# Kernel optimization log

Hardware: AMD Instinct MI355X
Metric: run time of the kernel (lower is better)

Reference implementation:

```python
import jax, jax.numpy as jnp
import numpy as np

TEMPERATURE = 0.07
C_MARGIN = 0.5
T_MARGIN = 1.0
GAMMA = 2.0
ALPHA = 0.25
SMOOTHING = 0.1
W_CONTRASTIVE = 0.1
W_TRIPLET = 0.1
W_FOCAL = 0.4
W_LABEL_SMOOTH = 0.4


def setup_inputs() -> dict:
    key = jax.random.key(0)
    k1, k2, k3 = jax.random.split(key, 3)
    B, C, D = 2048, 1000, 512
    pred = jax.random.normal(k1, (B, C), dtype=jnp.float32)
    target = jax.random.randint(k2, (B,), 0, C, dtype=jnp.int64)
    features = jax.random.normal(k3, (B, D), dtype=jnp.float32)
    return {"pred": pred, "target": target, "features": features}


def _safe_cdist(f):
    # Euclidean pairwise distance with zero-grad at zero distance (matches torch.cdist on diagonal).
    r = jnp.sum(f * f, axis=1)
    d2 = jnp.maximum(r[:, None] - 2.0 * (f @ f.T) + r[None, :], 0.0)
    pos = d2 > 0
    return jnp.sqrt(jnp.where(pos, d2, 1.0)) * pos


def _contrastive(features, labels):
    f = features / jnp.linalg.norm(features, axis=1, keepdims=True)
    sim = f @ f.T  # [B, B]
    lm = (labels[:, None] == labels[None, :]).astype(sim.dtype)
    pos = sim * lm
    pos_loss = -jnp.log(jnp.exp(pos / TEMPERATURE) + 1e-8)
    neg = sim * (1.0 - lm)
    neg_loss = jnp.maximum(C_MARGIN - neg, 0.0)
    return pos_loss.mean() + neg_loss.mean()


def _triplet(features, labels):
    B = features.shape[0]
    d = _safe_cdist(features)  # [B, B]
    lm = (labels[:, None] == labels[None, :]).astype(d.dtype)
    pm, nm = lm, 1.0 - lm

    def body(acc, args):
        di, pmi, nmi = args  # [B], [B], [B]
        # sum over (p, n): relu(d_ip - d_in + margin), masked
        contrib = jnp.sum(
            jnp.maximum(di[:, None] - di[None, :] + T_MARGIN, 0.0)
            * pmi[:, None] * nmi[None, :]
        )
        return acc + contrib, None

    loss, _ = jax.lax.scan(body, jnp.float32(0.0), (d, pm, nm))
    return loss / (B + 1e-8)


def _focal(pred, target):
    logp = jax.nn.log_softmax(pred, axis=1)
    ce = -jnp.take_along_axis(logp, target[:, None], axis=1)[:, 0]
    pt = jnp.exp(-ce)
    return (ALPHA * (1.0 - pt) ** GAMMA * ce).mean()


def _label_smoothing(pred, target):
    C = pred.shape[1]
    off = SMOOTHING / (C - 1)
    logp = jax.nn.log_softmax(pred, axis=1)
    # smooth target: off everywhere, (1 - smoothing) at target index
    tgt_logp = jnp.take_along_axis(logp, target[:, None], axis=1)[:, 0]
    loss = -(off * logp.sum(axis=1) + ((1.0 - SMOOTHING) - off) * tgt_logp)
    return loss.mean()


def reference(pred, target, features):
    lc = _contrastive(features, target)
    lt = _triplet(features, target)
    lf = _focal(pred, target)
    ls = _label_smoothing(pred, target)
    total = (W_CONTRASTIVE * lc + W_TRIPLET * lt
             + W_FOCAL * lf + W_LABEL_SMOOTH * ls)
    return jnp.stack([lc, lt, lf, ls, total])
```

## Files before the change

### kernel.cpp

```cpp
#include <hip/hip_runtime.h>
#include <hip/hip_bf16.h>
#include <math.h>

typedef __attribute__((ext_vector_type(8))) short bf16x8;
typedef __attribute__((ext_vector_type(4))) float f32x4;

static constexpr float TEMP_INV  = 1.0f / 0.07f;
static constexpr float C_MARGIN  = 0.5f;
static constexpr float T_MARGIN  = 1.0f;
static constexpr float ALPHA     = 0.25f;
static constexpr float SMOOTHING = 0.1f;
static constexpr float LSE_SHIFT = 8.0f;

__device__ __forceinline__ unsigned short f2bf(float x) {
    __hip_bfloat16 h = __float2bfloat16(x);
    return *reinterpret_cast<unsigned short*>(&h);
}
__device__ __forceinline__ float bf2f(unsigned short u) {
    union { unsigned int u32; float f; } U;
    U.u32 = ((unsigned int)u) << 16;
    return U.f;
}
__device__ __forceinline__ bf16x8 pack8(float4 a, float4 b) {
    bf16x8 r;
    r[0] = (short)f2bf(a.x); r[1] = (short)f2bf(a.y);
    r[2] = (short)f2bf(a.z); r[3] = (short)f2bf(a.w);
    r[4] = (short)f2bf(b.x); r[5] = (short)f2bf(b.y);
    r[6] = (short)f2bf(b.z); r[7] = (short)f2bf(b.w);
    return r;
}

__global__ __launch_bounds__(256) void gram_ce_kernel(
    const float* __restrict__ F, unsigned short* __restrict__ Gb,
    const float* __restrict__ pred, const int* __restrict__ target,
    float* __restrict__ partialCE, float* __restrict__ diag,
    float* __restrict__ inv_norm, int B, int D, int C, float off_const,
    int tilesX) {
    __shared__ unsigned short As[2][128 * 32];
    __shared__ unsigned short Bs[2][128 * 32];

    const int nTiles = tilesX * tilesX;
    const int tid = threadIdx.x;
    const int lane = tid & 63, wid = tid >> 6;

    if (blockIdx.x < nTiles) {
        const int b = blockIdx.x;
        const int x = b & 7, sq = x * 2 + ((b >> 3) >> 4);
        const int tis = (b >> 3) & 15;
        const int ti = (sq >> 2) * 4 + (tis >> 2);
        const int tj = (sq & 3) * 4 + (tis & 3);
        const int rowBase = ti * 128;
        const int colBase = tj * 128;
        const int wr = (wid >> 1) * 64;
        const int wc = (wid & 1) * 64;
        const int half = lane >> 4;
        const int rr   = lane & 15;

        const float* FA = F + (size_t)rowBase * D;
        const float* FB = F + (size_t)colBase * D;

        int ldo_[2]; size_t go_[2];
#pragma unroll
        for (int c = 0; c < 2; ++c) {
            const int chunk = c * 256 + tid;
            const int r2 = chunk >> 2, q = chunk & 3;
            ldo_[c] = r2 * 32 + ((q ^ (r2 & 3)) * 8);
            go_[c]  = (size_t)r2 * D + q * 8;
        }

        f32x4 acc[4][4];
#pragma unroll
        for (int m = 0; m < 4; ++m)
#pragma unroll
            for (int n = 0; n < 4; ++n) acc[m][n] = (f32x4){0.f, 0.f, 0.f, 0.f};

        float4 pa0[2], pa1[2], pb0[2], pb1[2];

#pragma unroll
        for (int c = 0; c < 2; ++c) {
            pa0[c] = *(const float4*)(FA + go_[c]);
            pa1[c] = *(const float4*)(FA + go_[c] + 4);
            pb0[c] = *(const float4*)(FB + go_[c]);
            pb1[c] = *(const float4*)(FB + go_[c] + 4);
        }
#pragma unroll
        for (int c = 0; c < 2; ++c) {
            *(bf16x8*)(&As[0][ldo_[c]]) = pack8(pa0[c], pa1[c]);
            *(bf16x8*)(&Bs[0][ldo_[c]]) = pack8(pb0[c], pb1[c]);
        }
        __syncthreads();

        const int NT = D / 32;
        for (int t = 0; t < NT; ++t) {
            const int cur = t & 1;
            if (t + 1 < NT) {
                const int k1 = (t + 1) * 32;
#pragma unroll
                for (int c = 0; c < 2; ++c) {
                    pa0[c] = *(const float4*)(FA + go_[c] + k1);
                    pa1[c] = *(const float4*)(FA + go_[c] + k1 + 4);
                    pb0[c] = *(const float4*)(FB + go_[c] + k1);
                    pb1[c] = *(const float4*)(FB + go_[c] + k1 + 4);
                }
            }
            bf16x8 af[4], bfv[4];
#pragma unroll
            for (int f = 0; f < 4; ++f) {
                const int ar = wr + f * 16 + rr;
                af[f]  = *(const bf16x8*)(&As[cur][ar * 32 + ((half ^ (ar & 3)) * 8)]);
                const int br = wc + f * 16 + rr;
                bfv[f] = *(const bf16x8*)(&Bs[cur][br * 32 + ((half ^ (br & 3)) * 8)]);
            }
#pragma unroll
            for (int m = 0; m < 4; ++m)
#pragma unroll
                for (int n = 0; n < 4; ++n)
                    acc[m][n] = __builtin_amdgcn_mfma_f32_16x16x32_bf16(
                        af[m], bfv[n], acc[m][n], 0, 0, 0);
            if (t + 1 < NT) {
#pragma unroll
                for (int c = 0; c < 2; ++c) {
                    *(bf16x8*)(&As[cur ^ 1][ldo_[c]]) = pack8(pa0[c], pa1[c]);
                    *(bf16x8*)(&Bs[cur ^ 1][ldo_[c]]) = pack8(pb0[c], pb1[c]);
                }
            }
            __syncthreads();
        }
#pragma unroll
        for (int m = 0; m < 4; ++m) {
            const int i0 = rowBase + wr + m * 16 + half * 4;
#pragma unroll
            for (int n = 0; n < 4; ++n) {
                const int j = colBase + wc + n * 16 + rr;
#pragma unroll
                for (int r = 0; r < 4; ++r)
                    Gb[(size_t)(i0 + r) * B + j] = f2bf(acc[m][n][r]);
            }
        }
    } else {
        const int i = (blockIdx.x - nTiles) * 4 + wid;
        const float4* Fr4 = (const float4*)(F + (size_t)i * D);
        float ns = 0.0f;
        for (int idx = lane; idx < (D >> 2); idx += 64) {
            float4 f = Fr4[idx];
            ns += f.x * f.x + f.y * f.y + f.z * f.z + f.w * f.w;
        }
        const float* prow = pred + (size_t)i * C;
        const float tlogit = prow[target[i]];
        const int Cv = C >> 2;
        float s = 0.0f, sp = 0.0f;
        for (int idx = lane; idx < Cv; idx += 64) {
            float4 v = ((const float4*)prow)[idx];
            s += __expf(v.x - LSE_SHIFT) + __expf(v.y - LSE_SHIFT)
               + __expf(v.z - LSE_SHIFT) + __expf(v.w - LSE_SHIFT);
            sp += v.x + v.y + v.z + v.w;
        }
        for (int j = Cv * 4 + lane; j < C; j += 64) {
            float v = prow[j];
            s += __expf(v - LSE_SHIFT);
            sp += v;
        }
#pragma unroll
        for (int off = 32; off > 0; off >>= 1) {
            s  += __shfl_down(s, off, 64);
            sp += __shfl_down(sp, off, 64);
            ns += __shfl_down(ns, off, 64);
        }
        if (lane == 0) {
            float lse = LSE_SHIFT + __logf(s);
            float tl  = tlogit - lse;
            float ce  = -tl;
            float pt  = __expf(tl);
            float omp = 1.0f - pt;
            float focal = ALPHA * omp * omp * ce;
            float sumlogp = sp - (float)C * lse;
            float lsv = -(off_const * sumlogp + ((1.0f - SMOOTHING) - off_const) * tl);
            partialCE[(size_t)i * 2]     = focal;
            partialCE[(size_t)i * 2 + 1] = lsv;
            diag[i] = ns;
            inv_norm[i] = 1.0f / sqrtf(ns);
        }
    }
}

__global__ __launch_bounds__(256) void row_loss_kernel(
    const unsigned short* __restrict__ Gb, const float* __restrict__ diag,
    const float* __restrict__ inv_norm, const int* __restrict__ labels,
    float* __restrict__ partial, int B) {
    __shared__ float p_d[256];
    __shared__ float red[12];
    __shared__ int p_cnt;
    const int tid = threadIdx.x;
    const int i = blockIdx.x;
    const int j0 = tid * 8;

    union { uint4 u; unsigned short s[8]; } GV;
    GV.u = *(const uint4*)(Gb + (size_t)i * B + j0);
    int lab[8];
    *(int4*)&lab[0] = *(const int4*)(labels + j0);
    *(int4*)&lab[4] = *(const int4*)(labels + j0 + 4);
    float dg[8], ivn[8];
    *(float4*)&dg[0]  = *(const float4*)(diag + j0);
    *(float4*)&dg[4]  = *(const float4*)(diag + j0 + 4);
    *(float4*)&ivn[0] = *(const float4*)(inv_norm + j0);
    *(float4*)&ivn[4] = *(const float4*)(inv_norm + j0 + 4);
    const int   li     = labels[i];
    const float ri     = diag[i];
    const float inv_ni = inv_norm[i];

    if (tid == 0) p_cnt = 0;
    __syncthreads();

    float pos = 0.0f, neg = 0.0f;
    float d8[8];
    int mmask = 0;
#pragma unroll
    for (int e = 0; e < 8; ++e) {
        const int j = j0 + e;
        const float g = bf2f(GV.s[e]);
        float sim = g * inv_ni * ivn[e];
        const float d2 = ri - 2.0f * g + dg[e];
        float d = (d2 > 0.0f) ? sqrtf(d2) : 0.0f;
        if (j == i) { sim = 1.0f; d = 0.0f; }
        d8[e] = d;
        if (lab[e] == li) {
            pos += -__logf(__expf(sim * TEMP_INV) + 1e-8f);
            neg += C_MARGIN;
            mmask |= (1 << e);
            int slot = atomicAdd(&p_cnt, 1);
            if (slot < 256) p_d[slot] = d;
        } else {
            neg += fmaxf(C_MARGIN - sim, 0.0f);
        }
    }
    __syncthreads();
    const int cnt = (p_cnt < 256) ? p_cnt : 256;
    float trip = 0.0f;
    for (int p = 0; p < cnt; ++p) {
        const float dp = p_d[p] + T_MARGIN;
#pragma unroll
        for (int e = 0; e < 8; ++e)
            if (!(mmask & (1 << e))) trip += fmaxf(dp - d8[e], 0.0f);
    }

    float r0 = pos, r1 = neg, r2 = trip;
#pragma unroll
    for (int off = 32; off > 0; off >>= 1) {
        r0 += __shfl_down(r0, off, 64);
        r1 += __shfl_down(r1, off, 64);
        r2 += __shfl_down(r2, off, 64);
    }
    const int lane = tid & 63, wid = tid >> 6;
    if (lane == 0) { red[wid] = r0; red[4 + wid] = r1; red[8 + wid] = r2; }
    __syncthreads();
    if (tid == 0) {
        float4 o;
        o.x = red[0] + red[1] + red[2] + red[3];
        o.y = red[4] + red[5] + red[6] + red[7];
        o.z = red[8] + red[9] + red[10] + red[11];
        o.w = 0.0f;
        *(float4*)(partial + (size_t)i * 4) = o;
    }
}

__global__ __launch_bounds__(1024) void reduce_kernel(
    const float* __restrict__ partialT, const float* __restrict__ partialCE,
    float* __restrict__ out, int B) {
    __shared__ float red[16][5];
    const int tid = threadIdx.x;
    float s[5] = {0.f, 0.f, 0.f, 0.f, 0.f};
    for (int r = tid; r < B; r += 1024) {
        float4 v = *(const float4*)(partialT + (size_t)r * 4);
        s[0] += v.x; s[1] += v.y; s[2] += v.z;
    }
    for (int t = tid; t < (B * 2) / 4; t += 1024) {
        float4 v = *(const float4*)(partialCE + (size_t)t * 4);
        s[3] += v.x + v.z; s[4] += v.y + v.w;
    }
#pragma unroll
    for (int off = 32; off > 0; off >>= 1) {
#pragma unroll
        for (int k = 0; k < 5; ++k) s[k] += __shfl_down(s[k], off, 64);
    }
    const int lane = tid & 63, wid = tid >> 6;
    if (lane == 0) {
#pragma unroll
        for (int k = 0; k < 5; ++k) red[wid][k] = s[k];
    }
    __syncthreads();
    if (tid == 0) {
        float t[5];
#pragma unroll
        for (int k = 0; k < 5; ++k) {
            t[k] = red[0][k];
#pragma unroll
            for (int q = 1; q < 16; ++q) t[k] += red[q][k];
        }
        double invB2 = 1.0 / ((double)B * (double)B);
        float lc = (float)(((double)t[0] + (double)t[1]) * invB2);
        float lt = (float)((double)t[2] / ((double)B + 1e-8));
        float lf = t[3] / (float)B;
        float ls = t[4] / (float)B;
        out[0] = lc;
        out[1] = lt;
        out[2] = lf;
        out[3] = ls;
        out[4] = 0.1f * lc + 0.1f * lt + 0.4f * lf + 0.4f * ls;
    }
}

extern "C" void kernel_launch(void* const* d_in, const int* in_sizes, int n_in,
                              void* d_out, int out_size, void* d_ws, size_t ws_size,
                              hipStream_t stream) {
    const float* pred     = (const float*)d_in[0];
    const int*   target   = (const int*)d_in[1];
    const float* features = (const float*)d_in[2];
    const int B = in_sizes[1];
    const int C = in_sizes[0] / B;
    const int D = in_sizes[2] / B;
    float* out = (float*)d_out;
    const int tilesX = B / 128;
    const int nTiles = tilesX * tilesX;

    float* partial   = (float*)d_ws;
    float* partialCE = partial + (size_t)B * 4;
    float* diag      = partialCE + (size_t)B * 2;
    float* inv_norm  = diag + B;
    unsigned short* Gb = (unsigned short*)(inv_norm + B);

    float off_const = SMOOTHING / (float)(C - 1);
    gram_ce_kernel<<<nTiles + B / 4, 256, 0, stream>>>(
        features, Gb, pred, target, partialCE, diag, inv_norm,
        B, D, C, off_const, tilesX);

    row_loss_kernel<<<B, 256, 0, stream>>>(Gb, diag, inv_norm, target,
                                           partial, B);

    reduce_kernel<<<1, 1024, 0, stream>>>(partial, partialCE, out, B);
}
```

Baseline: 31.17 us.

## Fuse norm, contrastive terms and distance computation into Gram GEMM epilogue

Each Gram tile now computes the squared row norms from the fp32 data it already loads for packing, then in the epilogue computes cosine similarity, the contrastive positive/negative sums and the Euclidean distance. It stores the bf16 distance matrix instead of the raw Gram matrix, with nontemporal stores. The row kernel now only does the triplet term and no longer reads diag/inv_norm arrays, and the separate norm pass in the CE blocks is removed. This moves transcendental work (exp, log, sqrt) into the GEMM blocks, adds shared-memory label/norm arrays and an extra block reduction there, and stores distance in bf16 rather than computing it from an fp32-derived Gram.

Result: slower. 37.99 us (+21.9%).

```diff
diff --git a/kernel.cpp b/kernel.cpp
--- a/kernel.cpp
+++ b/kernel.cpp
@@ -29,15 +29,20 @@
     r[6] = (short)f2bf(b.z); r[7] = (short)f2bf(b.w);
     return r;
 }
+__device__ __forceinline__ float dot4(float4 v) {
+    return v.x * v.x + v.y * v.y + v.z * v.z + v.w * v.w;
+}
 
 __global__ __launch_bounds__(256) void gram_ce_kernel(
-    const float* __restrict__ F, unsigned short* __restrict__ Gb,
+    const float* __restrict__ F, unsigned short* __restrict__ Gd,
     const float* __restrict__ pred, const int* __restrict__ target,
-    float* __restrict__ partialCE, float* __restrict__ diag,
-    float* __restrict__ inv_norm, int B, int D, int C, float off_const,
-    int tilesX) {
+    float* __restrict__ partialCE, float* __restrict__ partialPN,
+    int B, int D, int C, float off_const, int tilesX) {
     __shared__ unsigned short As[2][128 * 32];
     __shared__ unsigned short Bs[2][128 * 32];
+    __shared__ float rI[128], iI[128], rJ[128], iJ[128];
+    __shared__ int   labR[128], labC[128];
+    __shared__ float red[8];
 
     const int nTiles = tilesX * tilesX;
     const int tid = threadIdx.x;
@@ -59,6 +64,9 @@
         const float* FA = F + (size_t)rowBase * D;
         const float* FB = F + (size_t)colBase * D;
 
+        if (tid < 128) labR[tid] = target[rowBase + tid];
+        else           labC[tid - 128] = target[colBase + tid - 128];
+
         int ldo_[2]; size_t go_[2];
 #pragma unroll
         for (int c = 0; c < 2; ++c) {
@@ -74,6 +82,7 @@
 #pragma unroll
             for (int n = 0; n < 4; ++n) acc[m][n] = (f32x4){0.f, 0.f, 0.f, 0.f};
 
+        float nsA[2] = {0.f, 0.f}, nsB[2] = {0.f, 0.f};
         float4 pa0[2], pa1[2], pb0[2], pb1[2];
 
 #pragma unroll
@@ -87,6 +96,8 @@
         for (int c = 0; c < 2; ++c) {
             *(bf16x8*)(&As[0][ldo_[c]]) = pack8(pa0[c], pa1[c]);
             *(bf16x8*)(&Bs[0][ldo_[c]]) = pack8(pb0[c], pb1[c]);
+            nsA[c] += dot4(pa0[c]) + dot4(pa1[c]);
+            nsB[c] += dot4(pb0[c]) + dot4(pb1[c]);
         }
         __syncthreads();
 
@@ -122,29 +133,72 @@
                 for (int c = 0; c < 2; ++c) {
                     *(bf16x8*)(&As[cur ^ 1][ldo_[c]]) = pack8(pa0[c], pa1[c]);
                     *(bf16x8*)(&Bs[cur ^ 1][ldo_[c]]) = pack8(pb0[c], pb1[c]);
+                    nsA[c] += dot4(pa0[c]) + dot4(pa1[c]);
+                    nsB[c] += dot4(pb0[c]) + dot4(pb1[c]);
                 }
             }
             __syncthreads();
         }
+
+#pragma unroll
+        for (int c = 0; c < 2; ++c) {
+            float a = nsA[c], bb = nsB[c];
+            a  += __shfl_xor(a, 1, 64);  a  += __shfl_xor(a, 2, 64);
+            bb += __shfl_xor(bb, 1, 64); bb += __shfl_xor(bb, 2, 64);
+            if ((tid & 3) == 0) {
+                const int r = (c * 256 + tid) >> 2;
+                rI[r] = a;  iI[r] = 1.0f / sqrtf(a);
+                rJ[r] = bb; iJ[r] = 1.0f / sqrtf(bb);
+            }
+        }
+        __syncthreads();
+
+        float pos = 0.0f, neg = 0.0f;
+        int   jlab[4]; float jr[4], jij[4];
+#pragma unroll
+        for (int n = 0; n < 4; ++n) {
+            const int jl = wc + n * 16 + rr;
+            jlab[n] = labC[jl]; jr[n] = rJ[jl]; jij[n] = iJ[jl];
+        }
 #pragma unroll
         for (int m = 0; m < 4; ++m) {
-            const int i0 = rowBase + wr + m * 16 + half * 4;
-#pragma unroll
-            for (int n = 0; n < 4; ++n) {
-                const int j = colBase + wc + n * 16 + rr;
-#pragma unroll
-                for (int r = 0; r < 4; ++r)
-                    Gb[(size_t)(i0 + r) * B + j] = f2bf(acc[m][n][r]);
-            }
+#pragma unroll
+            for (int r = 0; r < 4; ++r) {
+                const int il = wr + m * 16 + half * 4 + r;
+                const int gi = rowBase + il;
+                const float ri_ = rI[il], ii = iI[il];
+                const int lr = labR[il];
+#pragma unroll
+                for (int n = 0; n < 4; ++n) {
+                    const int gj = colBase + wc + n * 16 + rr;
+                    const float g = acc[m][n][r];
+                    float sim = g * ii * jij[n];
+                    const float d2 = ri_ - 2.0f * g + jr[n];
+                    float d = (d2 > 0.0f) ? sqrtf(d2) : 0.0f;
+                    if (gi == gj) { sim = 1.0f; d = 0.0f; }
+                    if (lr == jlab[n]) {
+                        pos += -__logf(__expf(sim * TEMP_INV) + 1e-8f);
+                        neg += C_MARGIN;
+                    } else {
+                        neg += fmaxf(C_MARGIN - sim, 0.0f);
+                    }
+                    __builtin_nontemporal_store(f2bf(d), &Gd[(size_t)gi * B + gj]);
+                }
+            }
+        }
+#pragma unroll
+        for (int off = 32; off > 0; off >>= 1) {
+            pos += __shfl_down(pos, off, 64);
+            neg += __shfl_down(neg, off, 64);
+        }
+        if (lane == 0) { red[wid] = pos; red[4 + wid] = neg; }
+        __syncthreads();
+        if (tid == 0) {
+            partialPN[(size_t)b * 2]     = red[0] + red[1] + red[2] + red[3];
+            partialPN[(size_t)b * 2 + 1] = red[4] + red[5] + red[6] + red[7];
         }
     } else {
         const int i = (blockIdx.x - nTiles) * 4 + wid;
-        const float4* Fr4 = (const float4*)(F + (size_t)i * D);
-        float ns = 0.0f;
-        for (int idx = lane; idx < (D >> 2); idx += 64) {
-            float4 f = Fr4[idx];
-            ns += f.x * f.x + f.y * f.y + f.z * f.z + f.w * f.w;
-        }
         const float* prow = pred + (size_t)i * C;
         const float tlogit = prow[target[i]];
         const int Cv = C >> 2;
@@ -164,7 +218,6 @@
         for (int off = 32; off > 0; off >>= 1) {
             s  += __shfl_down(s, off, 64);
             sp += __shfl_down(sp, off, 64);
-            ns += __shfl_down(ns, off, 64);
         }
         if (lane == 0) {
             float lse = LSE_SHIFT + __logf(s);
@@ -177,60 +230,39 @@
             float lsv = -(off_const * sumlogp + ((1.0f - SMOOTHING) - off_const) * tl);
             partialCE[(size_t)i * 2]     = focal;
             partialCE[(size_t)i * 2 + 1] = lsv;
-            diag[i] = ns;
-            inv_norm[i] = 1.0f / sqrtf(ns);
         }
     }
 }
 
 __global__ __launch_bounds__(256) void row_loss_kernel(
-    const unsigned short* __restrict__ Gb, const float* __restrict__ diag,
-    const float* __restrict__ inv_norm, const int* __restrict__ labels,
+    const unsigned short* __restrict__ Gd, const int* __restrict__ labels,
     float* __restrict__ partial, int B) {
     __shared__ float p_d[256];
-    __shared__ float red[12];
+    __shared__ float red[4];
     __shared__ int p_cnt;
     const int tid = threadIdx.x;
     const int i = blockIdx.x;
     const int j0 = tid * 8;
 
     union { uint4 u; unsigned short s[8]; } GV;
-    GV.u = *(const uint4*)(Gb + (size_t)i * B + j0);
+    GV.u = *(const uint4*)(Gd + (size_t)i * B + j0);
     int lab[8];
     *(int4*)&lab[0] = *(const int4*)(labels + j0);
     *(int4*)&lab[4] = *(const int4*)(labels + j0 + 4);
-    float dg[8], ivn[8];
-    *(float4*)&dg[0]  = *(const float4*)(diag + j0);
-    *(float4*)&dg[4]  = *(const float4*)(diag + j0 + 4);
-    *(float4*)&ivn[0] = *(const float4*)(inv_norm + j0);
-    *(float4*)&ivn[4] = *(const float4*)(inv_norm + j0 + 4);
-    const int   li     = labels[i];
-    const float ri     = diag[i];
-    const float inv_ni = inv_norm[i];
+    const int li = labels[i];
 
     if (tid == 0) p_cnt = 0;
     __syncthreads();
 
-    float pos = 0.0f, neg = 0.0f;
     float d8[8];
     int mmask = 0;
 #pragma unroll
     for (int e = 0; e < 8; ++e) {
-        const int j = j0 + e;
-        const float g = bf2f(GV.s[e]);
-        float sim = g * inv_ni * ivn[e];
-        const float d2 = ri - 2.0f * g + dg[e];
-        float d = (d2 > 0.0f) ? sqrtf(d2) : 0.0f;
-        if (j == i) { sim = 1.0f; d = 0.0f; }
-        d8[e] = d;
+        d8[e] = bf2f(GV.s[e]);
         if (lab[e] == li) {
-            pos += -__logf(__expf(sim * TEMP_INV) + 1e-8f);
-            neg += C_MARGIN;
             mmask |= (1 << e);
             int slot = atomicAdd(&p_cnt, 1);
-            if (slot < 256) p_d[slot] = d;
-        } else {
-            neg += fmaxf(C_MARGIN - sim, 0.0f);
+            if (slot < 256) p_d[slot] = d8[e];
         }
     }
     __syncthreads();
@@ -243,35 +275,30 @@
             if (!(mmask & (1 << e))) trip += fmaxf(dp - d8[e], 0.0f);
     }
 
-    float r0 = pos, r1 = neg, r2 = trip;
-#pragma unroll
-    for (int off = 32; off > 0; off >>= 1) {
-        r0 += __shfl_down(r0, off, 64);
-        r1 += __shfl_down(r1, off, 64);
-        r2 += __shfl_down(r2, off, 64);
-    }
+#pragma unroll
+    for (int off = 32; off > 0; off >>= 1)
+        trip += __shfl_down(trip, off, 64);
     const int lane = tid & 63, wid = tid >> 6;
-    if (lane == 0) { red[wid] = r0; red[4 + wid] = r1; red[8 + wid] = r2; }
+    if (lane == 0) red[wid] = trip;
     __syncthreads();
-    if (tid == 0) {
-        float4 o;
-        o.x = red[0] + red[1] + red[2] + red[3];
-        o.y = red[4] + red[5] + red[6] + red[7];
-        o.z = red[8] + red[9] + red[10] + red[11];
-        o.w = 0.0f;
-        *(float4*)(partial + (size_t)i * 4) = o;
-    }
+    if (tid == 0)
+        partial[i] = red[0] + red[1] + red[2] + red[3];
 }
 
 __global__ __launch_bounds__(1024) void reduce_kernel(
-    const float* __restrict__ partialT, const float* __restrict__ partialCE,
-    float* __restrict__ out, int B) {
+    const float* __restrict__ partialT, const float* __restrict__ partialPN,
+    const float* __restrict__ partialCE, float* __restrict__ out,
+    int B, int nTiles) {
     __shared__ float red[16][5];
     const int tid = threadIdx.x;
     float s[5] = {0.f, 0.f, 0.f, 0.f, 0.f};
-    for (int r = tid; r < B; r += 1024) {
+    for (int t = tid; t < (nTiles * 2) / 4; t += 1024) {
+        float4 v = *(const float4*)(partialPN + (size_t)t * 4);
+        s[0] += v.x + v.z; s[1] += v.y + v.w;
+    }
+    for (int r = tid; r < B / 4; r += 1024) {
         float4 v = *(const float4*)(partialT + (size_t)r * 4);
-        s[0] += v.x; s[1] += v.y; s[2] += v.z;
+        s[2] += v.x + v.y + v.z + v.w;
     }
     for (int t = tid; t < (B * 2) / 4; t += 1024) {
         float4 v = *(const float4*)(partialCE + (size_t)t * 4);
@@ -323,18 +350,17 @@
     const int nTiles = tilesX * tilesX;
 
     float* partial   = (float*)d_ws;
-    float* partialCE = partial + (size_t)B * 4;
-    float* diag      = partialCE + (size_t)B * 2;
-    float* inv_norm  = diag + B;
-    unsigned short* Gb = (unsigned short*)(inv_norm + B);
+    float* partialPN = partial + B;
+    float* partialCE = partialPN + (size_t)nTiles * 2;
+    unsigned short* Gd = (unsigned short*)(partialCE + (size_t)B * 2);
 
     float off_const = SMOOTHING / (float)(C - 1);
     gram_ce_kernel<<<nTiles + B / 4, 256, 0, stream>>>(
-        features, Gb, pred, target, partialCE, diag, inv_norm,
+        features, Gd, pred, target, partialCE, partialPN,
         B, D, C, off_const, tilesX);
 
-    row_loss_kernel<<<B, 256, 0, stream>>>(Gb, diag, inv_norm, target,
-                                           partial, B);
-
-    reduce_kernel<<<1, 1024, 0, stream>>>(partial, partialCE, out, B);
-}
+    row_loss_kernel<<<B, 256, 0, stream>>>(Gd, target, partial, B);
+
+    reduce_kernel<<<1, 1024, 0, stream>>>(partial, partialPN, partialCE,
+                                          out, B, nTiles);
+}
```
